# Optimization experiments

Hardware: AMD Instinct MI355X
Metric: run time of the kernel (lower is better)

## Reference

```python
import jax, jax.numpy as jnp
import numpy as np

B, T, N, D = 4, 4, 256, 128  # batch, time_steps, num_nodes, features (in==out)
EPS = 1e-5
NEG = -1e9


def _glorot(key, shape):
    fan_in, fan_out = shape[0], shape[1]
    s = float(np.sqrt(6.0 / (fan_in + fan_out)))
    return jax.random.uniform(key, shape, jnp.float32, -s, s)


def setup_inputs() -> dict:
    key = jax.random.key(0)
    ks = jax.random.split(key, 8)
    x = jax.random.normal(ks[0], (B, T, N, D), jnp.float32)
    adj = (jax.random.uniform(ks[1], (N, N)) < 0.05).astype(jnp.float32)
    adj = jnp.maximum(adj, jnp.eye(N, dtype=jnp.float32))
    weight = _glorot(ks[2], (D, D))            # GCN weight [in, out]
    bias = jnp.zeros((D,), jnp.float32)
    att_w1 = _glorot(ks[3], (2 * D, D))        # Linear(2D -> D), column layout
    att_b1 = jnp.zeros((D,), jnp.float32)
    att_w2 = _glorot(ks[4], (D, 1))            # Linear(D -> 1)
    att_b2 = jnp.zeros((1,), jnp.float32)
    ln_gamma = jnp.ones((D,), jnp.float32)
    ln_beta = jnp.zeros((D,), jnp.float32)
    return dict(x=x, adj_matrix=adj, weight=weight, bias=bias,
                att_w1=att_w1, att_b1=att_b1, att_w2=att_w2, att_b2=att_b2,
                ln_gamma=ln_gamma, ln_beta=ln_beta)


def _layer_norm(y, gamma, beta):
    mu = jnp.mean(y, axis=-1, keepdims=True)
    var = jnp.mean(jnp.square(y - mu), axis=-1, keepdims=True)
    return (y - mu) * jax.lax.rsqrt(var + EPS) * gamma + beta


def reference(x, adj_matrix, weight, bias, att_w1, att_b1, att_w2, att_b2,
              ln_gamma, ln_beta):
    d_out = weight.shape[1]
    # split the first attention Linear so cat([h_i, h_j]) @ W1 == h_i@W1a + h_j@W1b
    W1a, W1b = att_w1[:d_out], att_w1[d_out:]
    w2 = att_w2[:, 0]
    mask = adj_matrix[None] == 0  # [1, N, N]

    def step(carry, x_t):  # x_t: [B, N, D]
        h = x_t @ weight + bias                                  # [B, N, D]
        a = h @ W1a                                              # [B, N, D]
        b = h @ W1b                                              # [B, N, D]
        # big intermediate the kernel would fuse away: [B, N, N, D]
        e = jax.nn.leaky_relu(a[:, :, None, :] + b[:, None, :, :] + att_b1, 0.2)
        scores = jnp.einsum('bijd,d->bij', e, w2) + att_b2[0]    # [B, N, N]
        scores = jnp.where(mask, NEG, scores)
        attn = jax.nn.softmax(scores, axis=-1)  # dropout is identity in eval
        agg = jnp.einsum('bij,bjd->bid', attn, h)                # [B, N, D]
        out = _layer_norm(agg + x_t, ln_gamma, ln_beta)          # in==out residual
        return carry, out

    _, ys = jax.lax.scan(step, None, jnp.swapaxes(x, 0, 1))      # [T, B, N, D]
    return jax.nn.relu(jnp.swapaxes(ys, 0, 1))                   # [B, T, N, D]
```

## Files before the change

kernel.cpp:

```cpp
#include <hip/hip_runtime.h>
#include <hip/hip_bf16.h>

#define BT 16
#define NN 256
#define DD 128
#define MROWS (BT*NN)

typedef __bf16 bf16x8 __attribute__((ext_vector_type(8)));
typedef float  f32x4  __attribute__((ext_vector_type(4)));

#define LREL(z) ((z) >= 0.0f ? (z) : 0.2f * (z))
#define HS_STRIDE 136

__global__ __launch_bounds__(256) void gemm2_kernel(
        const float* __restrict__ x, const float* __restrict__ weight,
        const float* __restrict__ bias, const float* __restrict__ attw1,
        const float* __restrict__ attb1,
        __bf16* __restrict__ hbuf, __bf16* __restrict__ abuf,
        __bf16* __restrict__ bbuf) {
    int tid = threadIdx.x;
    int w = tid >> 6, l = tid & 63;
    int chunk = blockIdx.x >> 1, parity = blockIdx.x & 1;
    int row0 = chunk * 16;
    int lrow = l & 15, lk8 = (l >> 4) * 8;

    __shared__ __align__(16) __bf16 hs[16][HS_STRIDE];

    const float* abase = x + (size_t)(row0 + lrow) * DD + lk8;
    bf16x8 af[4];
#pragma unroll
    for (int kt = 0; kt < 4; ++kt) {
        float4 u0 = *(const float4*)(abase + 32 * kt);
        float4 u1 = *(const float4*)(abase + 32 * kt + 4);
        af[kt][0]=(__bf16)u0.x; af[kt][1]=(__bf16)u0.y;
        af[kt][2]=(__bf16)u0.z; af[kt][3]=(__bf16)u0.w;
        af[kt][4]=(__bf16)u1.x; af[kt][5]=(__bf16)u1.y;
        af[kt][6]=(__bf16)u1.z; af[kt][7]=(__bf16)u1.w;
    }

#pragma unroll
    for (int s = 0; s < 2; ++s) {
        int n0 = (w + 4 * s) * 16;
        int ncol = n0 + lrow;
        bf16x8 wf[4];
#pragma unroll
        for (int kt = 0; kt < 4; ++kt) {
            const float* wp = weight + (size_t)(lk8 + 32 * kt) * DD + ncol;
#pragma unroll
            for (int j = 0; j < 8; ++j)
                wf[kt][j] = (__bf16)wp[(size_t)j * DD];
        }
        f32x4 acc = {0.f, 0.f, 0.f, 0.f};
        acc = __builtin_amdgcn_mfma_f32_16x16x32_bf16(af[0], wf[0], acc, 0, 0, 0);
        acc = __builtin_amdgcn_mfma_f32_16x16x32_bf16(af[1], wf[1], acc, 0, 0, 0);
        acc = __builtin_amdgcn_mfma_f32_16x16x32_bf16(af[2], wf[2], acc, 0, 0, 0);
        acc = __builtin_amdgcn_mfma_f32_16x16x32_bf16(af[3], wf[3], acc, 0, 0, 0);

        float bb = bias[ncol];
        int rloc = (l >> 4) * 4;
        __bf16* hout = hbuf + (size_t)(row0 + rloc) * DD + ncol;
#pragma unroll
        for (int r = 0; r < 4; ++r) {
            __bf16 hv = (__bf16)(acc[r] + bb);
            hs[rloc + r][ncol] = hv;
            if (parity == 0) hout[(size_t)r * DD] = hv;
        }
    }
    __syncthreads();

    bf16x8 ha[4];
#pragma unroll
    for (int kt = 0; kt < 4; ++kt)
        ha[kt] = *(const bf16x8*)(&hs[lrow][lk8 + 32 * kt]);

#pragma unroll
    for (int s = 0; s < 2; ++s) {
        int n0 = (w + 4 * s) * 16;
        int ncol = n0 + lrow;
        bf16x8 w1f[4];
#pragma unroll
        for (int kt = 0; kt < 4; ++kt) {
            const float* wp = attw1 + (size_t)(parity * DD + lk8 + 32 * kt) * DD + ncol;
#pragma unroll
            for (int j = 0; j < 8; ++j)
                w1f[kt][j] = (__bf16)wp[(size_t)j * DD];
        }
        f32x4 acc = {0.f, 0.f, 0.f, 0.f};
        acc = __builtin_amdgcn_mfma_f32_16x16x32_bf16(ha[0], w1f[0], acc, 0, 0, 0);
        acc = __builtin_amdgcn_mfma_f32_16x16x32_bf16(ha[1], w1f[1], acc, 0, 0, 0);
        acc = __builtin_amdgcn_mfma_f32_16x16x32_bf16(ha[2], w1f[2], acc, 0, 0, 0);
        acc = __builtin_amdgcn_mfma_f32_16x16x32_bf16(ha[3], w1f[3], acc, 0, 0, 0);

        float bb = parity ? attb1[ncol] : 0.f;
        __bf16* dst = (parity ? bbuf : abuf) + (size_t)(row0 + (l >> 4) * 4) * DD + ncol;
#pragma unroll
        for (int r = 0; r < 4; ++r)
            dst[(size_t)r * DD] = (__bf16)(acc[r] + bb);
    }
}

__global__ __launch_bounds__(256) void attn_kernel(
        const __bf16* __restrict__ hbuf, const __bf16* __restrict__ abuf,
        const __bf16* __restrict__ bbuf, const float* __restrict__ x,
        const float* __restrict__ adj, const float* __restrict__ w2,
        const float* __restrict__ gamma, const float* __restrict__ beta,
        float* __restrict__ out) {
    int tid = threadIdx.x;
    int w = tid >> 6, l = tid & 63;
    int i  = (blockIdx.x & 63) * 4 + w;
    int bt = blockIdx.x >> 6;

    __shared__ int nbr_l[4][64];

    int cnt = 0;
    const float* adjrow = adj + (size_t)i * NN;
    for (int jt = 0; jt < NN / 64; ++jt) {
        int j = jt * 64 + l;
        float v = adjrow[j];
        unsigned long long mask = __ballot(v != 0.f);
        if (v != 0.f) {
            int pos = cnt + __popcll(mask & ((1ull << l) - 1ull));
            if (pos < 64) nbr_l[w][pos] = j;
        }
        cnt += __popcll(mask);
    }
    cnt = min(cnt, 64);
    int jreg = nbr_l[w][l];

    const __bf16* arow = abuf + (size_t)(bt * NN + i) * DD;
    float a0 = (float)arow[l], a1 = (float)arow[l + 64];
    float w20 = w2[l],  w21 = w2[l + 64];
    const __bf16* bbase = bbuf + (size_t)bt * NN * DD;

    float m = -3.0e38f, myp = 0.f;
    int c = 0;
    for (; c + 3 < cnt; c += 4) {
        int j0 = __shfl(jreg, c);
        int j1 = __shfl(jreg, c + 1);
        int j2 = __shfl(jreg, c + 2);
        int j3 = __shfl(jreg, c + 3);
        const __bf16* B0 = bbase + (size_t)j0 * DD;
        const __bf16* B1 = bbase + (size_t)j1 * DD;
        const __bf16* B2 = bbase + (size_t)j2 * DD;
        const __bf16* B3 = bbase + (size_t)j3 * DD;
        float p0 = LREL(a0 + (float)B0[l]) * w20 + LREL(a1 + (float)B0[l + 64]) * w21;
        float p1 = LREL(a0 + (float)B1[l]) * w20 + LREL(a1 + (float)B1[l + 64]) * w21;
        float p2 = LREL(a0 + (float)B2[l]) * w20 + LREL(a1 + (float)B2[l + 64]) * w21;
        float p3 = LREL(a0 + (float)B3[l]) * w20 + LREL(a1 + (float)B3[l + 64]) * w21;
#pragma unroll
        for (int off = 32; off; off >>= 1) {
            p0 += __shfl_xor(p0, off);
            p1 += __shfl_xor(p1, off);
            p2 += __shfl_xor(p2, off);
            p3 += __shfl_xor(p3, off);
        }
        myp = (l == c)     ? p0 : myp;
        myp = (l == c + 1) ? p1 : myp;
        myp = (l == c + 2) ? p2 : myp;
        myp = (l == c + 3) ? p3 : myp;
        m = fmaxf(m, fmaxf(fmaxf(p0, p1), fmaxf(p2, p3)));
    }
    for (; c < cnt; ++c) {
        int j0 = __shfl(jreg, c);
        const __bf16* B0 = bbase + (size_t)j0 * DD;
        float p0 = LREL(a0 + (float)B0[l]) * w20 + LREL(a1 + (float)B0[l + 64]) * w21;
#pragma unroll
        for (int off = 32; off; off >>= 1) p0 += __shfl_xor(p0, off);
        myp = (l == c) ? p0 : myp;
        m = fmaxf(m, p0);
    }

    float wgt = (l < cnt) ? __expf(myp - m) : 0.f;
    float dsum = wgt;
#pragma unroll
    for (int off = 32; off; off >>= 1) dsum += __shfl_xor(dsum, off);
    float inv = 1.f / dsum;

    const __bf16* hbase = hbuf + (size_t)bt * NN * DD;
    float acc0 = 0.f, acc1 = 0.f;
    c = 0;
    for (; c + 3 < cnt; c += 4) {
        float wc0 = __shfl(wgt, c),     wc1 = __shfl(wgt, c + 1);
        float wc2 = __shfl(wgt, c + 2), wc3 = __shfl(wgt, c + 3);
        int j0 = __shfl(jreg, c),     j1 = __shfl(jreg, c + 1);
        int j2 = __shfl(jreg, c + 2), j3 = __shfl(jreg, c + 3);
        const __bf16* H0 = hbase + (size_t)j0 * DD;
        const __bf16* H1 = hbase + (size_t)j1 * DD;
        const __bf16* H2 = hbase + (size_t)j2 * DD;
        const __bf16* H3 = hbase + (size_t)j3 * DD;
        acc0 += wc0 * (float)H0[l]      + wc1 * (float)H1[l]
              + wc2 * (float)H2[l]      + wc3 * (float)H3[l];
        acc1 += wc0 * (float)H0[l + 64] + wc1 * (float)H1[l + 64]
              + wc2 * (float)H2[l + 64] + wc3 * (float)H3[l + 64];
    }
    for (; c < cnt; ++c) {
        float wc = __shfl(wgt, c);
        int j = __shfl(jreg, c);
        const __bf16* H = hbase + (size_t)j * DD;
        acc0 += wc * (float)H[l];
        acc1 += wc * (float)H[l + 64];
    }

    const float* xrow = x + (size_t)(bt * NN + i) * DD;
    float y0 = acc0 * inv + xrow[l];
    float y1 = acc1 * inv + xrow[l + 64];

    float s = y0 + y1;
#pragma unroll
    for (int off = 32; off; off >>= 1) s += __shfl_xor(s, off);
    float mu = s * (1.0f / 128.0f);
    float v0 = y0 - mu, v1 = y1 - mu;
    float vs = v0 * v0 + v1 * v1;
#pragma unroll
    for (int off = 32; off; off >>= 1) vs += __shfl_xor(vs, off);
    float rstd = rsqrtf(vs * (1.0f / 128.0f) + 1e-5f);

    float o0 = v0 * rstd * gamma[l]      + beta[l];
    float o1 = v1 * rstd * gamma[l + 64] + beta[l + 64];

    float* orow = out + (size_t)(bt * NN + i) * DD;
    orow[l]      = fmaxf(o0, 0.0f);
    orow[l + 64] = fmaxf(o1, 0.0f);
}

extern "C" void kernel_launch(void* const* d_in, const int* in_sizes, int n_in,
                              void* d_out, int out_size, void* d_ws, size_t ws_size,
                              hipStream_t stream) {
    const float* x      = (const float*)d_in[0];
    const float* adj    = (const float*)d_in[1];
    const float* weight = (const float*)d_in[2];
    const float* bias   = (const float*)d_in[3];
    const float* attw1  = (const float*)d_in[4];
    const float* attb1  = (const float*)d_in[5];
    const float* attw2  = (const float*)d_in[6];
    const float* gamma  = (const float*)d_in[8];
    const float* beta   = (const float*)d_in[9];
    float* out = (float*)d_out;

    char* p = (char*)d_ws;
    __bf16* hbuf = (__bf16*)p;        p += (size_t)MROWS * DD * 2;
    __bf16* abuf = (__bf16*)p;        p += (size_t)MROWS * DD * 2;
    __bf16* bbuf = (__bf16*)p;

    gemm2_kernel<<<MROWS / 16 * 2, 256, 0, stream>>>(x, weight, bias, attw1, attb1,
                                                     hbuf, abuf, bbuf);
    attn_kernel<<<NN / 4 * BT, 256, 0, stream>>>(hbuf, abuf, bbuf, x, adj,
                                                 attw2, gamma, beta, out);
}
```

Baseline: 26.97 us.

## Fuse projection GEMMs and sparse attention into one kernel with LDS-resident h and b

Replaces the two-kernel pipeline with a single fused kernel. Each 512-thread block recomputes h and the b projection for a full 256-node (b,t) slice into LDS, computes the a projection only for its 16 query rows, then runs the neighbour-gather attention, softmax, residual and LayerNorm directly from LDS. This drops the global round trip of the h/a/b intermediates and one kernel launch. In exchange, the h and W1b GEMMs for each slice are recomputed 16 times (once per block), each block needs about 140KB of LDS, and the grid shrinks to 256 blocks of 512 threads.

```diff
diff --git a/kernel.cpp b/kernel.cpp
--- a/kernel.cpp
+++ b/kernel.cpp
@@ -4,44 +4,50 @@
 #define BT 16
 #define NN 256
 #define DD 128
-#define MROWS (BT*NN)
+#define HSS 136
 
 typedef __bf16 bf16x8 __attribute__((ext_vector_type(8)));
 typedef float  f32x4  __attribute__((ext_vector_type(4)));
 
 #define LREL(z) ((z) >= 0.0f ? (z) : 0.2f * (z))
-#define HS_STRIDE 136
-
-__global__ __launch_bounds__(256) void gemm2_kernel(
-        const float* __restrict__ x, const float* __restrict__ weight,
-        const float* __restrict__ bias, const float* __restrict__ attw1,
-        const float* __restrict__ attb1,
-        __bf16* __restrict__ hbuf, __bf16* __restrict__ abuf,
-        __bf16* __restrict__ bbuf) {
+
+#define LDS_BYTES ((256 + 256 + 16) * HSS * 2 + 8 * 64 * 4)
+
+__global__ __launch_bounds__(512, 1) void fused_kernel(
+        const float* __restrict__ x, const float* __restrict__ adj,
+        const float* __restrict__ weight, const float* __restrict__ bias,
+        const float* __restrict__ attw1, const float* __restrict__ attb1,
+        const float* __restrict__ w2, const float* __restrict__ gamma,
+        const float* __restrict__ beta, float* __restrict__ out) {
+    extern __shared__ char smem[];
+    __bf16* hs  = (__bf16*)smem;
+    __bf16* bs  = hs + 256 * HSS;
+    __bf16* as_ = bs + 256 * HSS;
+    int*    nbr = (int*)(as_ + 16 * HSS);
+
     int tid = threadIdx.x;
     int w = tid >> 6, l = tid & 63;
-    int chunk = blockIdx.x >> 1, parity = blockIdx.x & 1;
-    int row0 = chunk * 16;
+    int grp = blockIdx.x & 15, bt = blockIdx.x >> 4;
     int lrow = l & 15, lk8 = (l >> 4) * 8;
-
-    __shared__ __align__(16) __bf16 hs[16][HS_STRIDE];
-
-    const float* abase = x + (size_t)(row0 + lrow) * DD + lk8;
-    bf16x8 af[4];
-#pragma unroll
-    for (int kt = 0; kt < 4; ++kt) {
-        float4 u0 = *(const float4*)(abase + 32 * kt);
-        float4 u1 = *(const float4*)(abase + 32 * kt + 4);
-        af[kt][0]=(__bf16)u0.x; af[kt][1]=(__bf16)u0.y;
-        af[kt][2]=(__bf16)u0.z; af[kt][3]=(__bf16)u0.w;
-        af[kt][4]=(__bf16)u1.x; af[kt][5]=(__bf16)u1.y;
-        af[kt][6]=(__bf16)u1.z; af[kt][7]=(__bf16)u1.w;
-    }
-
-#pragma unroll
-    for (int s = 0; s < 2; ++s) {
-        int n0 = (w + 4 * s) * 16;
-        int ncol = n0 + lrow;
+    int rsub = (l >> 4) * 4;
+
+    bf16x8 af[2][4];
+#pragma unroll
+    for (int rt2 = 0; rt2 < 2; ++rt2) {
+        const float* abase = x + ((size_t)bt * NN + (2 * w + rt2) * 16 + lrow) * DD + lk8;
+#pragma unroll
+        for (int kt = 0; kt < 4; ++kt) {
+            float4 u0 = *(const float4*)(abase + 32 * kt);
+            float4 u1 = *(const float4*)(abase + 32 * kt + 4);
+            af[rt2][kt][0]=(__bf16)u0.x; af[rt2][kt][1]=(__bf16)u0.y;
+            af[rt2][kt][2]=(__bf16)u0.z; af[rt2][kt][3]=(__bf16)u0.w;
+            af[rt2][kt][4]=(__bf16)u1.x; af[rt2][kt][5]=(__bf16)u1.y;
+            af[rt2][kt][6]=(__bf16)u1.z; af[rt2][kt][7]=(__bf16)u1.w;
+        }
+    }
+#pragma unroll
+    for (int ct = 0; ct < 8; ++ct) {
+        int ncol = ct * 16 + lrow;
         bf16x8 wf[4];
 #pragma unroll
         for (int kt = 0; kt < 4; ++kt) {
@@ -50,177 +56,193 @@
             for (int j = 0; j < 8; ++j)
                 wf[kt][j] = (__bf16)wp[(size_t)j * DD];
         }
-        f32x4 acc = {0.f, 0.f, 0.f, 0.f};
-        acc = __builtin_amdgcn_mfma_f32_16x16x32_bf16(af[0], wf[0], acc, 0, 0, 0);
-        acc = __builtin_amdgcn_mfma_f32_16x16x32_bf16(af[1], wf[1], acc, 0, 0, 0);
-        acc = __builtin_amdgcn_mfma_f32_16x16x32_bf16(af[2], wf[2], acc, 0, 0, 0);
-        acc = __builtin_amdgcn_mfma_f32_16x16x32_bf16(af[3], wf[3], acc, 0, 0, 0);
-
         float bb = bias[ncol];
-        int rloc = (l >> 4) * 4;
-        __bf16* hout = hbuf + (size_t)(row0 + rloc) * DD + ncol;
-#pragma unroll
-        for (int r = 0; r < 4; ++r) {
-            __bf16 hv = (__bf16)(acc[r] + bb);
-            hs[rloc + r][ncol] = hv;
-            if (parity == 0) hout[(size_t)r * DD] = hv;
+#pragma unroll
+        for (int rt2 = 0; rt2 < 2; ++rt2) {
+            f32x4 acc = {0.f, 0.f, 0.f, 0.f};
+            acc = __builtin_amdgcn_mfma_f32_16x16x32_bf16(af[rt2][0], wf[0], acc, 0, 0, 0);
+            acc = __builtin_amdgcn_mfma_f32_16x16x32_bf16(af[rt2][1], wf[1], acc, 0, 0, 0);
+            acc = __builtin_amdgcn_mfma_f32_16x16x32_bf16(af[rt2][2], wf[2], acc, 0, 0, 0);
+            acc = __builtin_amdgcn_mfma_f32_16x16x32_bf16(af[rt2][3], wf[3], acc, 0, 0, 0);
+            int row0 = (2 * w + rt2) * 16 + rsub;
+#pragma unroll
+            for (int r = 0; r < 4; ++r)
+                hs[(size_t)(row0 + r) * HSS + ncol] = (__bf16)(acc[r] + bb);
         }
     }
     __syncthreads();
 
-    bf16x8 ha[4];
-#pragma unroll
-    for (int kt = 0; kt < 4; ++kt)
-        ha[kt] = *(const bf16x8*)(&hs[lrow][lk8 + 32 * kt]);
-
-#pragma unroll
-    for (int s = 0; s < 2; ++s) {
-        int n0 = (w + 4 * s) * 16;
-        int ncol = n0 + lrow;
+    bf16x8 ha[2][4];
+#pragma unroll
+    for (int rt2 = 0; rt2 < 2; ++rt2)
+#pragma unroll
+        for (int kt = 0; kt < 4; ++kt)
+            ha[rt2][kt] = *(const bf16x8*)&hs[(size_t)((2 * w + rt2) * 16 + lrow) * HSS
+                                             + lk8 + 32 * kt];
+#pragma unroll
+    for (int ct = 0; ct < 8; ++ct) {
+        int ncol = ct * 16 + lrow;
         bf16x8 w1f[4];
 #pragma unroll
         for (int kt = 0; kt < 4; ++kt) {
-            const float* wp = attw1 + (size_t)(parity * DD + lk8 + 32 * kt) * DD + ncol;
+            const float* wp = attw1 + (size_t)(DD + lk8 + 32 * kt) * DD + ncol;
 #pragma unroll
             for (int j = 0; j < 8; ++j)
                 w1f[kt][j] = (__bf16)wp[(size_t)j * DD];
         }
+        float bb = attb1[ncol];
+#pragma unroll
+        for (int rt2 = 0; rt2 < 2; ++rt2) {
+            f32x4 acc = {0.f, 0.f, 0.f, 0.f};
+            acc = __builtin_amdgcn_mfma_f32_16x16x32_bf16(ha[rt2][0], w1f[0], acc, 0, 0, 0);
+            acc = __builtin_amdgcn_mfma_f32_16x16x32_bf16(ha[rt2][1], w1f[1], acc, 0, 0, 0);
+            acc = __builtin_amdgcn_mfma_f32_16x16x32_bf16(ha[rt2][2], w1f[2], acc, 0, 0, 0);
+            acc = __builtin_amdgcn_mfma_f32_16x16x32_bf16(ha[rt2][3], w1f[3], acc, 0, 0, 0);
+            int row0 = (2 * w + rt2) * 16 + rsub;
+#pragma unroll
+            for (int r = 0; r < 4; ++r)
+                bs[(size_t)(row0 + r) * HSS + ncol] = (__bf16)(acc[r] + bb);
+        }
+    }
+    {
+        bf16x8 ho[4];
+#pragma unroll
+        for (int kt = 0; kt < 4; ++kt)
+            ho[kt] = *(const bf16x8*)&hs[(size_t)(grp * 16 + lrow) * HSS + lk8 + 32 * kt];
+        int ncol = w * 16 + lrow;
+        bf16x8 w1f[4];
+#pragma unroll
+        for (int kt = 0; kt < 4; ++kt) {
+            const float* wp = attw1 + (size_t)(lk8 + 32 * kt) * DD + ncol;
+#pragma unroll
+            for (int j = 0; j < 8; ++j)
+                w1f[kt][j] = (__bf16)wp[(size_t)j * DD];
+        }
         f32x4 acc = {0.f, 0.f, 0.f, 0.f};
-        acc = __builtin_amdgcn_mfma_f32_16x16x32_bf16(ha[0], w1f[0], acc, 0, 0, 0);
-        acc = __builtin_amdgcn_mfma_f32_16x16x32_bf16(ha[1], w1f[1], acc, 0, 0, 0);
-        acc = __builtin_amdgcn_mfma_f32_16x16x32_bf16(ha[2], w1f[2], acc, 0, 0, 0);
-        acc = __builtin_amdgcn_mfma_f32_16x16x32_bf16(ha[3], w1f[3], acc, 0, 0, 0);
-
-        float bb = parity ? attb1[ncol] : 0.f;
-        __bf16* dst = (parity ? bbuf : abuf) + (size_t)(row0 + (l >> 4) * 4) * DD + ncol;
+        acc = __builtin_amdgcn_mfma_f32_16x16x32_bf16(ho[0], w1f[0], acc, 0, 0, 0);
+        acc = __builtin_amdgcn_mfma_f32_16x16x32_bf16(ho[1], w1f[1], acc, 0, 0, 0);
+        acc = __builtin_amdgcn_mfma_f32_16x16x32_bf16(ho[2], w1f[2], acc, 0, 0, 0);
+        acc = __builtin_amdgcn_mfma_f32_16x16x32_bf16(ho[3], w1f[3], acc, 0, 0, 0);
 #pragma unroll
         for (int r = 0; r < 4; ++r)
-            dst[(size_t)r * DD] = (__bf16)(acc[r] + bb);
-    }
-}
-
-__global__ __launch_bounds__(256) void attn_kernel(
-        const __bf16* __restrict__ hbuf, const __bf16* __restrict__ abuf,
-        const __bf16* __restrict__ bbuf, const float* __restrict__ x,
-        const float* __restrict__ adj, const float* __restrict__ w2,
-        const float* __restrict__ gamma, const float* __restrict__ beta,
-        float* __restrict__ out) {
-    int tid = threadIdx.x;
-    int w = tid >> 6, l = tid & 63;
-    int i  = (blockIdx.x & 63) * 4 + w;
-    int bt = blockIdx.x >> 6;
-
-    __shared__ int nbr_l[4][64];
-
-    int cnt = 0;
-    const float* adjrow = adj + (size_t)i * NN;
-    for (int jt = 0; jt < NN / 64; ++jt) {
-        int j = jt * 64 + l;
-        float v = adjrow[j];
-        unsigned long long mask = __ballot(v != 0.f);
-        if (v != 0.f) {
-            int pos = cnt + __popcll(mask & ((1ull << l) - 1ull));
-            if (pos < 64) nbr_l[w][pos] = j;
-        }
-        cnt += __popcll(mask);
-    }
-    cnt = min(cnt, 64);
-    int jreg = nbr_l[w][l];
-
-    const __bf16* arow = abuf + (size_t)(bt * NN + i) * DD;
-    float a0 = (float)arow[l], a1 = (float)arow[l + 64];
-    float w20 = w2[l],  w21 = w2[l + 64];
-    const __bf16* bbase = bbuf + (size_t)bt * NN * DD;
-
-    float m = -3.0e38f, myp = 0.f;
-    int c = 0;
-    for (; c + 3 < cnt; c += 4) {
-        int j0 = __shfl(jreg, c);
-        int j1 = __shfl(jreg, c + 1);
-        int j2 = __shfl(jreg, c + 2);
-        int j3 = __shfl(jreg, c + 3);
-        const __bf16* B0 = bbase + (size_t)j0 * DD;
-        const __bf16* B1 = bbase + (size_t)j1 * DD;
-        const __bf16* B2 = bbase + (size_t)j2 * DD;
-        const __bf16* B3 = bbase + (size_t)j3 * DD;
-        float p0 = LREL(a0 + (float)B0[l]) * w20 + LREL(a1 + (float)B0[l + 64]) * w21;
-        float p1 = LREL(a0 + (float)B1[l]) * w20 + LREL(a1 + (float)B1[l + 64]) * w21;
-        float p2 = LREL(a0 + (float)B2[l]) * w20 + LREL(a1 + (float)B2[l + 64]) * w21;
-        float p3 = LREL(a0 + (float)B3[l]) * w20 + LREL(a1 + (float)B3[l + 64]) * w21;
-#pragma unroll
-        for (int off = 32; off; off >>= 1) {
-            p0 += __shfl_xor(p0, off);
-            p1 += __shfl_xor(p1, off);
-            p2 += __shfl_xor(p2, off);
-            p3 += __shfl_xor(p3, off);
-        }
-        myp = (l == c)     ? p0 : myp;
-        myp = (l == c + 1) ? p1 : myp;
-        myp = (l == c + 2) ? p2 : myp;
-        myp = (l == c + 3) ? p3 : myp;
-        m = fmaxf(m, fmaxf(fmaxf(p0, p1), fmaxf(p2, p3)));
-    }
-    for (; c < cnt; ++c) {
-        int j0 = __shfl(jreg, c);
-        const __bf16* B0 = bbase + (size_t)j0 * DD;
-        float p0 = LREL(a0 + (float)B0[l]) * w20 + LREL(a1 + (float)B0[l + 64]) * w21;
-#pragma unroll
-        for (int off = 32; off; off >>= 1) p0 += __shfl_xor(p0, off);
-        myp = (l == c) ? p0 : myp;
-        m = fmaxf(m, p0);
-    }
-
-    float wgt = (l < cnt) ? __expf(myp - m) : 0.f;
-    float dsum = wgt;
-#pragma unroll
-    for (int off = 32; off; off >>= 1) dsum += __shfl_xor(dsum, off);
-    float inv = 1.f / dsum;
-
-    const __bf16* hbase = hbuf + (size_t)bt * NN * DD;
-    float acc0 = 0.f, acc1 = 0.f;
-    c = 0;
-    for (; c + 3 < cnt; c += 4) {
-        float wc0 = __shfl(wgt, c),     wc1 = __shfl(wgt, c + 1);
-        float wc2 = __shfl(wgt, c + 2), wc3 = __shfl(wgt, c + 3);
-        int j0 = __shfl(jreg, c),     j1 = __shfl(jreg, c + 1);
-        int j2 = __shfl(jreg, c + 2), j3 = __shfl(jreg, c + 3);
-        const __bf16* H0 = hbase + (size_t)j0 * DD;
-        const __bf16* H1 = hbase + (size_t)j1 * DD;
-        const __bf16* H2 = hbase + (size_t)j2 * DD;
-        const __bf16* H3 = hbase + (size_t)j3 * DD;
-        acc0 += wc0 * (float)H0[l]      + wc1 * (float)H1[l]
-              + wc2 * (float)H2[l]      + wc3 * (float)H3[l];
-        acc1 += wc0 * (float)H0[l + 64] + wc1 * (float)H1[l + 64]
-              + wc2 * (float)H2[l + 64] + wc3 * (float)H3[l + 64];
-    }
-    for (; c < cnt; ++c) {
-        float wc = __shfl(wgt, c);
-        int j = __shfl(jreg, c);
-        const __bf16* H = hbase + (size_t)j * DD;
-        acc0 += wc * (float)H[l];
-        acc1 += wc * (float)H[l + 64];
-    }
-
-    const float* xrow = x + (size_t)(bt * NN + i) * DD;
-    float y0 = acc0 * inv + xrow[l];
-    float y1 = acc1 * inv + xrow[l + 64];
-
-    float s = y0 + y1;
-#pragma unroll
-    for (int off = 32; off; off >>= 1) s += __shfl_xor(s, off);
-    float mu = s * (1.0f / 128.0f);
-    float v0 = y0 - mu, v1 = y1 - mu;
-    float vs = v0 * v0 + v1 * v1;
-#pragma unroll
-    for (int off = 32; off; off >>= 1) vs += __shfl_xor(vs, off);
-    float rstd = rsqrtf(vs * (1.0f / 128.0f) + 1e-5f);
-
-    float o0 = v0 * rstd * gamma[l]      + beta[l];
-    float o1 = v1 * rstd * gamma[l + 64] + beta[l + 64];
-
-    float* orow = out + (size_t)(bt * NN + i) * DD;
-    orow[l]      = fmaxf(o0, 0.0f);
-    orow[l + 64] = fmaxf(o1, 0.0f);
+            as_[(size_t)(rsub + r) * HSS + ncol] = (__bf16)acc[r];
+    }
+    __syncthreads();
+
+    float w20 = w2[l], w21 = w2[l + 64];
+    float gm0 = gamma[l], gm1 = gamma[l + 64];
+    float be0 = beta[l], be1 = beta[l + 64];
+
+#pragma unroll
+    for (int rep = 0; rep < 2; ++rep) {
+        int iloc = w * 2 + rep;
+        int i = grp * 16 + iloc;
+
+        int cnt = 0;
+        const float* adjrow = adj + (size_t)i * NN;
+        for (int jt = 0; jt < NN / 64; ++jt) {
+            int j = jt * 64 + l;
+            float v = adjrow[j];
+            unsigned long long mask = __ballot(v != 0.f);
+            if (v != 0.f) {
+                int pos = cnt + __popcll(mask & ((1ull << l) - 1ull));
+                if (pos < 64) nbr[w * 64 + pos] = j;
+            }
+            cnt += __popcll(mask);
+        }
+        cnt = min(cnt, 64);
+        int jreg = nbr[w * 64 + l];
+
+        float a0 = (float)as_[(size_t)iloc * HSS + l];
+        float a1 = (float)as_[(size_t)iloc * HSS + l + 64];
+
+        float m = -3.0e38f, myp = 0.f;
+        int c = 0;
+        for (; c + 3 < cnt; c += 4) {
+            int j0 = __shfl(jreg, c),     j1 = __shfl(jreg, c + 1);
+            int j2 = __shfl(jreg, c + 2), j3 = __shfl(jreg, c + 3);
+            const __bf16* B0 = bs + (size_t)j0 * HSS;
+            const __bf16* B1 = bs + (size_t)j1 * HSS;
+            const __bf16* B2 = bs + (size_t)j2 * HSS;
+            const __bf16* B3 = bs + (size_t)j3 * HSS;
+            float p0 = LREL(a0 + (float)B0[l]) * w20 + LREL(a1 + (float)B0[l + 64]) * w21;
+            float p1 = LREL(a0 + (float)B1[l]) * w20 + LREL(a1 + (float)B1[l + 64]) * w21;
+            float p2 = LREL(a0 + (float)B2[l]) * w20 + LREL(a1 + (float)B2[l + 64]) * w21;
+            float p3 = LREL(a0 + (float)B3[l]) * w20 + LREL(a1 + (float)B3[l + 64]) * w21;
+#pragma unroll
+            for (int off = 32; off; off >>= 1) {
+                p0 += __shfl_xor(p0, off);
+                p1 += __shfl_xor(p1, off);
+                p2 += __shfl_xor(p2, off);
+                p3 += __shfl_xor(p3, off);
+            }
+            myp = (l == c)     ? p0 : myp;
+            myp = (l == c + 1) ? p1 : myp;
+            myp = (l == c + 2) ? p2 : myp;
+            myp = (l == c + 3) ? p3 : myp;
+            m = fmaxf(m, fmaxf(fmaxf(p0, p1), fmaxf(p2, p3)));
+        }
+        for (; c < cnt; ++c) {
+            int j0 = __shfl(jreg, c);
+            const __bf16* B0 = bs + (size_t)j0 * HSS;
+            float p0 = LREL(a0 + (float)B0[l]) * w20 + LREL(a1 + (float)B0[l + 64]) * w21;
+#pragma unroll
+            for (int off = 32; off; off >>= 1) p0 += __shfl_xor(p0, off);
+            myp = (l == c) ? p0 : myp;
+            m = fmaxf(m, p0);
+        }
+
+        float wgt = (l < cnt) ? __expf(myp - m) : 0.f;
+        float dsum = wgt;
+#pragma unroll
+        for (int off = 32; off; off >>= 1) dsum += __shfl_xor(dsum, off);
+        float inv = 1.f / dsum;
+
+        float acc0 = 0.f, acc1 = 0.f;
+        c = 0;
+        for (; c + 3 < cnt; c += 4) {
+            float wc0 = __shfl(wgt, c),     wc1 = __shfl(wgt, c + 1);
+            float wc2 = __shfl(wgt, c + 2), wc3 = __shfl(wgt, c + 3);
+            int j0 = __shfl(jreg, c),     j1 = __shfl(jreg, c + 1);
+            int j2 = __shfl(jreg, c + 2), j3 = __shfl(jreg, c + 3);
+            const __bf16* H0 = hs + (size_t)j0 * HSS;
+            const __bf16* H1 = hs + (size_t)j1 * HSS;
+            const __bf16* H2 = hs + (size_t)j2 * HSS;
+            const __bf16* H3 = hs + (size_t)j3 * HSS;
+            acc0 += wc0 * (float)H0[l]      + wc1 * (float)H1[l]
+                  + wc2 * (float)H2[l]      + wc3 * (float)H3[l];
+            acc1 += wc0 * (float)H0[l + 64] + wc1 * (float)H1[l + 64]
+                  + wc2 * (float)H2[l + 64] + wc3 * (float)H3[l + 64];
+        }
+        for (; c < cnt; ++c) {
+            float wc = __shfl(wgt, c);
+            int j = __shfl(jreg, c);
+            const __bf16* H = hs + (size_t)j * HSS;
+            acc0 += wc * (float)H[l];
+            acc1 += wc * (float)H[l + 64];
+        }
+
+        const float* xrow = x + ((size_t)bt * NN + i) * DD;
+        float y0 = acc0 * inv + xrow[l];
+        float y1 = acc1 * inv + xrow[l + 64];
+
+        float s = y0 + y1;
+#pragma unroll
+        for (int off = 32; off; off >>= 1) s += __shfl_xor(s, off);
+        float mu = s * (1.0f / 128.0f);
+        float v0 = y0 - mu, v1 = y1 - mu;
+        float vs = v0 * v0 + v1 * v1;
+#pragma unroll
+        for (int off = 32; off; off >>= 1) vs += __shfl_xor(vs, off);
+        float rstd = rsqrtf(vs * (1.0f / 128.0f) + 1e-5f);
+
+        float o0 = v0 * rstd * gm0 + be0;
+        float o1 = v1 * rstd * gm1 + be1;
+
+        float* orow = out + ((size_t)bt * NN + i) * DD;
+        orow[l]      = fmaxf(o0, 0.0f);
+        orow[l + 64] = fmaxf(o1, 0.0f);
+    }
 }
 
 extern "C" void kernel_launch(void* const* d_in, const int* in_sizes, int n_in,
@@ -237,13 +259,6 @@
     const float* beta   = (const float*)d_in[9];
     float* out = (float*)d_out;
 
-    char* p = (char*)d_ws;
-    __bf16* hbuf = (__bf16*)p;        p += (size_t)MROWS * DD * 2;
-    __bf16* abuf = (__bf16*)p;        p += (size_t)MROWS * DD * 2;
-    __bf16* bbuf = (__bf16*)p;
-
-    gemm2_kernel<<<MROWS / 16 * 2, 256, 0, stream>>>(x, weight, bias, attw1, attb1,
-                                                     hbuf, abuf, bbuf);
-    attn_kernel<<<NN / 4 * BT, 256, 0, stream>>>(hbuf, abuf, bbuf, x, adj,
-                                                 attw2, gamma, beta, out);
+    fused_kernel<<<BT * 16, 512, LDS_BYTES, stream>>>(
+        x, adj, weight, bias, attw1, attb1, attw2, gamma, beta, out);
 }
```

Measured after the change: 30.92 us. 1.15x slower.
